# Performance work log

Hardware: AMD Instinct MI355X
Metric: run time of the kernel (lower is better)

Reference implementation:

```python
import math
import jax, jax.numpy as jnp
import numpy as np

N_HEADS = 12


def _rel_to_abs(x):
    # x: [b, h, L, 2L-1] relative logits -> [b, h, L, L] absolute-position scores
    b, h, L, _ = x.shape
    x = jnp.pad(x, ((0, 0), (0, 0), (0, 0), (0, 1)))           # [b,h,L,2L]
    xf = x.reshape(b, h, L * 2 * L)
    xf = jnp.pad(xf, ((0, 0), (0, 0), (0, L - 1)))
    return xf.reshape(b, h, L + 1, 2 * L - 1)[:, :, :L, L - 1:]


def _abs_to_rel(x):
    # x: [b, h, L, L] attention weights -> [b, h, L, 2L-1] relative-position weights
    b, h, L, _ = x.shape
    x = jnp.pad(x, ((0, 0), (0, 0), (0, 0), (0, L - 1)))        # [b,h,L,2L-1]
    xf = x.reshape(b, h, L * (2 * L - 1))
    xf = jnp.pad(xf, ((0, 0), (0, 0), (L, 0)))
    return xf.reshape(b, h, L, 2 * L)[:, :, :, 1:]


def _get_relative_embeddings(emb, length):
    # emb: [n_rel, 2*window+1, k] -> [n_rel, 2*length-1, k]
    window = (emb.shape[1] - 1) // 2
    pad_len = max(length - (window + 1), 0)
    start = max(window + 1 - length, 0)
    if pad_len > 0:
        emb = jnp.pad(emb, ((0, 0), (pad_len, pad_len), (0, 0)))
    return emb[:, start:start + 2 * length - 1]


def setup_inputs() -> dict:
    key = jax.random.key(0)
    ks = jax.random.split(key, 8)
    B, C, T, H = 4, 768, 1024, N_HEADS
    K = C // H
    W = 10
    xavier = math.sqrt(2.0 / (C + C))          # xavier_uniform std analogue
    rel_std = K ** (-0.5)
    return {
        "x": jax.random.normal(ks[0], (B, C, T), jnp.float32),
        "c": jax.random.normal(ks[1], (B, C, T), jnp.float32),
        "Wq": jax.random.normal(ks[2], (C, C), jnp.float32) * xavier,
        "bq": jnp.zeros((C,), jnp.float32),
        "Wk": jax.random.normal(ks[3], (C, C), jnp.float32) * xavier,
        "bk": jnp.zeros((C,), jnp.float32),
        "Wv": jax.random.normal(ks[4], (C, C), jnp.float32) * xavier,
        "bv": jnp.zeros((C,), jnp.float32),
        "Wo": jax.random.normal(ks[5], (C, C), jnp.float32) * xavier,
        "bo": jnp.zeros((C,), jnp.float32),
        "emb_rel_k": jax.random.normal(ks[6], (1, 2 * W + 1, K), jnp.float32) * rel_std,
        "emb_rel_v": jax.random.normal(ks[7], (1, 2 * W + 1, K), jnp.float32) * rel_std,
    }


def reference(x, c, Wq, bq, Wk, bk, Wv, bv, Wo, bo, emb_rel_k, emb_rel_v):
    B, C, T = x.shape
    H = N_HEADS
    K = C // H

    def proj(W_, b_, inp):  # Conv1d(kernel=1) == channel-wise linear
        return jnp.einsum('oi,bit->bot', W_, inp) + b_[None, :, None]

    # [B,C,T] -> [B,H,T,K]
    q = proj(Wq, bq, x).reshape(B, H, K, T).transpose(0, 1, 3, 2)
    k = proj(Wk, bk, c).reshape(B, H, K, T).transpose(0, 1, 3, 2)
    v = proj(Wv, bv, c).reshape(B, H, K, T).transpose(0, 1, 3, 2)

    qs = q * (1.0 / math.sqrt(K))
    scores = jnp.einsum('bhtd,bhsd->bhts', qs, k)               # [B,H,T,T]

    # relative key logits via skewing trick
    rel_k = _get_relative_embeddings(emb_rel_k, T)              # [1,2T-1,K]
    rel_logits = jnp.einsum('bhtd,md->bhtm', qs, rel_k[0])      # [B,H,T,2T-1]
    scores = scores + _rel_to_abs(rel_logits)

    # proximal bias: -log(1 + |i - j|)
    r = jnp.arange(T, dtype=scores.dtype)
    scores = scores - jnp.log1p(jnp.abs(r[None, :] - r[:, None]))[None, None]

    p = jax.nn.softmax(scores, axis=-1)
    out = jnp.einsum('bhts,bhsd->bhtd', p, v)                   # [B,H,T,K]

    # relative value contribution
    rel_v = _get_relative_embeddings(emb_rel_v, T)              # [1,2T-1,K]
    out = out + jnp.einsum('bhtm,md->bhtd', _abs_to_rel(p), rel_v[0])

    out = out.transpose(0, 1, 3, 2).reshape(B, C, T)            # [B,C,T]
    return jnp.einsum('oi,bit->bot', Wo, out) + bo[None, :, None]
```

## Files before the change

### kernel.cpp

```cpp
#include <hip/hip_runtime.h>
#include <hip/hip_bf16.h>

using bf16 = __hip_bfloat16;
typedef __attribute__((ext_vector_type(8))) short short8;
typedef __attribute__((ext_vector_type(4))) float f32x4;

static constexpr int C = 768, T = 1024, H = 12, D = 64;

__device__ __forceinline__ f32x4 mfma16(short8 a, short8 b, f32x4 c){
  return __builtin_amdgcn_mfma_f32_16x16x32_bf16(a, b, c, 0, 0, 0);
}

__device__ __forceinline__ void gload16(const void* g, void* l){
  void* gv = const_cast<void*>(g);
  __builtin_amdgcn_global_load_lds((__attribute__((address_space(1))) void*)gv,
                                   (__attribute__((address_space(3))) void*)l, 16, 0, 0);
}

__device__ __forceinline__ float b2f(short s){
  unsigned u = ((unsigned)(unsigned short)s) << 16;
  return __builtin_bit_cast(float, u);
}

__device__ __forceinline__ int cvtpk(float a, float b){
  int r;
  asm("v_cvt_pk_bf16_f32 %0, %1, %2" : "=v"(r) : "v"(a), "v"(b));
  return r;
}

union PkU { int i[4]; short8 v; };

__global__ __launch_bounds__(256) void prep_kernel(const float* __restrict__ xin,
    const float* __restrict__ cin, const float* __restrict__ Wq,
    const float* __restrict__ Wk, const float* __restrict__ Wv,
    const float* __restrict__ Wo, bf16* __restrict__ xo, bf16* __restrict__ co,
    bf16* __restrict__ wq, bf16* __restrict__ wk, bf16* __restrict__ wv,
    bf16* __restrict__ wo){
  const int z = blockIdx.z;
  if (z < 8){
    __shared__ float tile[64][65];
    const int b = z & 3, which = z >> 2;
    const float* in = which ? cin : xin;
    bf16* out = which ? co : xo;
    const int t0 = blockIdx.x*64, c0 = blockIdx.y*64;
    const int u = threadIdx.x & 63, r0 = threadIdx.x >> 6;
    const float* ip = in + ((size_t)b*C + c0)*T + t0;
    #pragma unroll
    for (int i = r0; i < 64; i += 4) tile[i][u] = ip[(size_t)i*T + u];
    __syncthreads();
    bf16* op = out + ((size_t)b*T + t0)*C + c0;
    #pragma unroll
    for (int j = r0; j < 64; j += 4) op[(size_t)j*C + u] = (bf16)tile[u][j];
  } else {
    const int chunk = (z - 8)*192 + blockIdx.y*16 + blockIdx.x;
    const int m = chunk / 576;
    const int off = (chunk % 576)*1024 + threadIdx.x*4;
    const float* in = m==0 ? Wq : m==1 ? Wk : m==2 ? Wv : Wo;
    bf16* out = m==0 ? wq : m==1 ? wk : m==2 ? wv : wo;
    float4 v = *(const float4*)(in + off);
    out[off+0] = (bf16)v.x; out[off+1] = (bf16)v.y;
    out[off+2] = (bf16)v.z; out[off+3] = (bf16)v.w;
  }
}

__global__ __launch_bounds__(256,3) void gemm_qkv(const bf16* __restrict__ xb,
    const bf16* __restrict__ cb, const bf16* __restrict__ wq, const bf16* __restrict__ wk,
    const bf16* __restrict__ wv, const float* __restrict__ bq, const float* __restrict__ bk,
    const float* __restrict__ bv, bf16* __restrict__ qout, bf16* __restrict__ kout,
    bf16* __restrict__ vout){
  const int tid = threadIdx.x, lane = tid & 63, w = tid >> 6;
  const int wr = w >> 1, wc = w & 1, g = lane >> 4, cl = lane & 15;
  const int bz = blockIdx.y, b = bz & 3, mode = bz >> 2;
  const int lb = blockIdx.x;
  int m0, n0;
  if (mode == 2){ m0 = (lb >> 3)*128; n0 = (lb & 7)*128; }
  else          { m0 = (lb & 7)*128;  n0 = (lb >> 3)*128; }
  const bf16* A  = (mode==0) ? xb + (size_t)b*T*C : (mode==1) ? cb + (size_t)b*T*C : wv;
  const bf16* Bp = (mode==2) ? cb + (size_t)b*T*C : (mode==0) ? wq : wk;
  const float* bias = (mode==0) ? bq : (mode==1) ? bk : bv;
  const float scale = (mode==0) ? 0.125f*1.44269504088896f : 1.0f;
  __shared__ bf16 lA[128*64], lB[128*64];
  f32x4 acc[4][4] = {};
  const bf16* Ars = A  + (size_t)m0*768;
  const bf16* Brs = Bp + (size_t)n0*768;
  for (int k0 = 0; k0 < 768; k0 += 64){
    __syncthreads();
    #pragma unroll
    for (int rr = 0; rr < 4; ++rr){
      const int u = rr*256 + tid;
      const int row = u >> 3, cc = u & 7;
      const int src = row*768 + k0 + ((cc ^ (row & 7))*8);
      gload16(Ars + src, &lA[(size_t)u*8]);
      gload16(Brs + src, &lB[(size_t)u*8]);
    }
    __syncthreads();
    #pragma unroll
    for (int kh = 0; kh < 2; ++kh){
      short8 af[4], bfr[4];
      #pragma unroll
      for (int mi = 0; mi < 4; ++mi){
        const int row = wr*64 + mi*16 + cl;
        af[mi] = *(const short8*)&lA[row*64 + (((g + kh*4) ^ (row & 7))*8)];
      }
      #pragma unroll
      for (int ni = 0; ni < 4; ++ni){
        const int row = wc*64 + ni*16 + cl;
        bfr[ni] = *(const short8*)&lB[row*64 + (((g + kh*4) ^ (row & 7))*8)];
      }
      __builtin_amdgcn_s_setprio(1);
      #pragma unroll
      for (int mi = 0; mi < 4; ++mi)
        #pragma unroll
        for (int ni = 0; ni < 4; ++ni)
          acc[mi][ni] = mfma16(af[mi], bfr[ni], acc[mi][ni]);
      __builtin_amdgcn_s_setprio(0);
    }
  }
  #pragma unroll
  for (int mi = 0; mi < 4; ++mi){
    const int mB = m0 + wr*64 + mi*16 + g*4;
    #pragma unroll
    for (int ni = 0; ni < 4; ++ni){
      const int n = n0 + wc*64 + ni*16 + cl;
      #pragma unroll
      for (int r = 0; r < 4; ++r){
        const int m = mB + r;
        float v = acc[mi][ni][r];
        if (mode <= 1){
          v = (v + bias[n]) * scale;
          bf16* outp = mode ? kout : qout;
          outp[(size_t)b*(H*T*D) + (size_t)(n >> 6)*(T*D) + (size_t)m*D + (n & 63)] = (bf16)v;
        } else {
          v += bias[m];
          vout[(size_t)b*(C*T) + (size_t)m*T + n] = (bf16)v;
        }
      }
    }
  }
}

__global__ __launch_bounds__(256,3) void gemm_o(const bf16* __restrict__ wo,
                                                const bf16* __restrict__ attn,
                                                const float* __restrict__ bias,
                                                float* __restrict__ outp){
  const int tid = threadIdx.x, lane = tid & 63, w = tid >> 6;
  const int wr = w >> 1, wc = w & 1, g = lane >> 4, cl = lane & 15;
  const int b = blockIdx.z;
  const int q = blockIdx.y*6 + blockIdx.x;
  const int m0 = (q >> 3)*128, n0 = (q & 7)*128;
  __shared__ bf16 lA[128*64], lB[128*64];
  f32x4 acc[4][4] = {};
  const bf16* Ars = wo + (size_t)m0*768;
  const bf16* Brs = attn + (size_t)b*T*C + (size_t)n0*768;
  for (int k0 = 0; k0 < 768; k0 += 64){
    __syncthreads();
    #pragma unroll
    for (int rr = 0; rr < 4; ++rr){
      const int u = rr*256 + tid;
      const int row = u >> 3, cc = u & 7;
      const int src = row*768 + k0 + ((cc ^ (row & 7))*8);
      gload16(Ars + src, &lA[(size_t)u*8]);
      gload16(Brs + src, &lB[(size_t)u*8]);
    }
    __syncthreads();
    #pragma unroll
    for (int kh = 0; kh < 2; ++kh){
      short8 af[4], bfr[4];
      #pragma unroll
      for (int mi = 0; mi < 4; ++mi){
        const int row = wr*64 + mi*16 + cl;
        af[mi] = *(const short8*)&lA[row*64 + (((g + kh*4) ^ (row & 7))*8)];
      }
      #pragma unroll
      for (int ni = 0; ni < 4; ++ni){
        const int row = wc*64 + ni*16 + cl;
        bfr[ni] = *(const short8*)&lB[row*64 + (((g + kh*4) ^ (row & 7))*8)];
      }
      __builtin_amdgcn_s_setprio(1);
      #pragma unroll
      for (int mi = 0; mi < 4; ++mi)
        #pragma unroll
        for (int ni = 0; ni < 4; ++ni)
          acc[mi][ni] = mfma16(af[mi], bfr[ni], acc[mi][ni]);
      __builtin_amdgcn_s_setprio(0);
    }
  }
  #pragma unroll
  for (int mi = 0; mi < 4; ++mi){
    const int mB = m0 + wr*64 + mi*16 + g*4;
    #pragma unroll
    for (int ni = 0; ni < 4; ++ni){
      const int n = n0 + wc*64 + ni*16 + cl;
      #pragma unroll
      for (int r = 0; r < 4; ++r){
        const int m = mB + r;
        outp[(size_t)b*(C*T) + (size_t)m*T + n] = acc[mi][ni][r] + bias[m];
      }
    }
  }
}

__global__ __launch_bounds__(256,4) void attn_kernel(const bf16* __restrict__ qws,
                                                     const bf16* __restrict__ kws,
                                                     const bf16* __restrict__ vws,
                                                     bf16* __restrict__ aws,
                                                     const float* __restrict__ relk,
                                                     const float* __restrict__ relv){
  const int tid = threadIdx.x, lane = tid & 63, w = tid >> 6;
  const int g = lane >> 4, cl = lane & 15;
  const int i0 = blockIdx.y*64, bh = blockIdx.x;
  const int b = bh / H, h = bh % H;
  const int ql = w*16 + cl;
  const int qt = i0 + ql;

  __shared__ __align__(16) char smem[40960];
  bf16*  lKV   = (bf16*)smem;
  float* bandS = (float*)(smem + 32768);
  bf16*  relkD = (bf16*)(smem + 38144);
  bf16*  lEmb32 = lKV + 4096;
  bf16*  lEV    = lKV;
  bf16*  lQ     = lKV + 3*4096;

  const bf16* qg = qws + ((size_t)bh*T + i0)*D;
  const bf16* kg = kws + (size_t)bh*T*D;
  const bf16* vg = vws + ((size_t)b*C + h*D)*T;

  int kOff[2], vOff[2], qOff[2], dst[2];
  #pragma unroll
  for (int r = 0; r < 2; ++r){
    const int u = r*256 + tid, L = u >> 3, cc = u & 7;
    const int sc8 = (cc ^ (L & 7))*8;
    const int sig = (((L>>4)&1)<<5) | (((L>>2)&3)<<3) | (((L>>5)&1)<<2) | (L&3);
    kOff[r] = sig*64 + sc8;
    vOff[r] = L*T + sc8;
    qOff[r] = L*64 + sc8;
    dst[r]  = u*8;
  }

  #pragma unroll
  for (int r = 0; r < 2; ++r){
    gload16(qg + qOff[r], &lQ[dst[r]]);
    gload16(kg + kOff[r], &lKV[dst[r]]);
    gload16(vg + vOff[r], &lKV[2*4096 + dst[r]]);
  }
  for (int idx = tid; idx < 2048; idx += 256){
    const int row = idx >> 6, col = idx & 63;
    const float v = (row < 21) ? relk[idx] : 0.0f;
    lEmb32[row*64 + (((col >> 3) ^ (row & 7))*8) + (col & 7)] = (bf16)v;
  }
  __syncthreads();

  const short8 aq0 = *(const short8*)&lQ[ql*64 + ((g ^ (ql & 7))*8)];
  const short8 aq1 = *(const short8*)&lQ[ql*64 + (((g + 4) ^ (ql & 7))*8)];

  #pragma unroll
  for (int ni2 = 0; ni2 < 2; ++ni2){
    const int row = ni2*16 + cl;
    short8 e0 = *(const short8*)&lEmb32[row*64 + ((g ^ (row & 7))*8)];
    short8 e1 = *(const short8*)&lEmb32[row*64 + (((g + 4) ^ (row & 7))*8)];
    f32x4 rk = {};
    rk = mfma16(e0, aq0, rk);
    rk = mfma16(e1, aq1, rk);
    #pragma unroll
    for (int rr = 0; rr < 4; ++rr){
      const int ridx = ni2*16 + 4*g + rr;
      if (ridx < 21) relkD[ql*22 + ridx] = (bf16)rk[rr];
    }
  }
  __syncthreads();

  float mreg = -1e30f, lreg = 0.f;
  f32x4 o[4] = {};
  const int koffA[4] = {8*g, 32 + 8*g, 4 + 8*g, 36 + 8*g};

  for (int jt = 0; jt < 16; ++jt){
    const int j0 = jt*64, cur = jt & 1, nxt = cur ^ 1;
    if (jt < 15){
      const int jn = j0 + 64;
      #pragma unroll
      for (int r = 0; r < 2; ++r){
        gload16(kg + jn*64 + kOff[r], &lKV[nxt*4096 + dst[r]]);
        gload16(vg + jn + vOff[r],    &lKV[(2 + nxt)*4096 + dst[r]]);
      }
      asm volatile("s_waitcnt vmcnt(4)" ::: "memory");
    } else {
      asm volatile("s_waitcnt vmcnt(0)" ::: "memory");
    }
    asm volatile("s_barrier" ::: "memory");

    const bf16* Kc = lKV + cur*4096;
    const bf16* Vc = lKV + (2 + cur)*4096;

    f32x4 s[4] = {};
    __builtin_amdgcn_s_setprio(1);
    #pragma unroll
    for (int ni = 0; ni < 4; ++ni){
      const int row = ni*16 + cl;
      short8 k0f = *(const short8*)&Kc[row*64 + ((g ^ (row & 7))*8)];
      s[ni] = mfma16(k0f, aq0, s[ni]);
      short8 k1f = *(const short8*)&Kc[row*64 + (((g + 4) ^ (row & 7))*8)];
      s[ni] = mfma16(k1f, aq1, s[ni]);
    }
    __builtin_amdgcn_s_setprio(0);

    const int dj = j0 - i0;
    if (dj == 0 || dj == 64 || dj == -64){
      #pragma unroll
      for (int ni = 0; ni < 4; ++ni){
        const int ibase = j0 + koffA[ni] - qt;
        #pragma unroll
        for (int r = 0; r < 4; ++r){
          const int dd = ibase + r;
          float v = s[ni][r] - __log2f(fabsf((float)dd) + 1.0f);
          if ((unsigned)(dd + 10) <= 20u){
            v += b2f(*(const short*)&relkD[ql*22 + dd + 10]);
            bandS[ql*21 + dd + 10] = v;
          }
          s[ni][r] = v;
        }
      }
    } else {
      #pragma unroll
      for (int ni = 0; ni < 4; ++ni){
        const float fb = (float)(j0 + koffA[ni] - qt);
        #pragma unroll
        for (int r = 0; r < 4; ++r)
          s[ni][r] -= __log2f(fabsf(fb + (float)r) + 1.0f);
      }
    }

    float m0 = fmaxf(fmaxf(s[0][0], s[0][1]), fmaxf(s[0][2], s[0][3]));
    float m1 = fmaxf(fmaxf(s[1][0], s[1][1]), fmaxf(s[1][2], s[1][3]));
    float m2 = fmaxf(fmaxf(s[2][0], s[2][1]), fmaxf(s[2][2], s[2][3]));
    float m3 = fmaxf(fmaxf(s[3][0], s[3][1]), fmaxf(s[3][2], s[3][3]));
    float mx = fmaxf(fmaxf(m0, m1), fmaxf(m2, m3));
    mx = fmaxf(mx, __shfl_xor(mx, 16));
    mx = fmaxf(mx, __shfl_xor(mx, 32));
    if (!__all(mx <= mreg + 8.0f)){
      const float mn = fmaxf(mreg, mx);
      const float sc = __builtin_amdgcn_exp2f(mreg - mn);
      lreg *= sc;
      #pragma unroll
      for (int di = 0; di < 4; ++di)
        #pragma unroll
        for (int r = 0; r < 4; ++r) o[di][r] *= sc;
      mreg = mn;
    }
    float rs = 0.f;
    #pragma unroll
    for (int ni = 0; ni < 4; ++ni)
      #pragma unroll
      for (int r = 0; r < 4; ++r){
        float p = __builtin_amdgcn_exp2f(s[ni][r] - mreg);
        s[ni][r] = p; rs += p;
      }
    rs += __shfl_xor(rs, 16);
    rs += __shfl_xor(rs, 32);
    lreg += rs;

    PkU bf0, bf1;
    bf0.i[0] = cvtpk(s[0][0], s[0][1]); bf0.i[1] = cvtpk(s[0][2], s[0][3]);
    bf0.i[2] = cvtpk(s[2][0], s[2][1]); bf0.i[3] = cvtpk(s[2][2], s[2][3]);
    bf1.i[0] = cvtpk(s[1][0], s[1][1]); bf1.i[1] = cvtpk(s[1][2], s[1][3]);
    bf1.i[2] = cvtpk(s[3][0], s[3][1]); bf1.i[3] = cvtpk(s[3][2], s[3][3]);

    __builtin_amdgcn_s_setprio(1);
    #pragma unroll
    for (int di = 0; di < 4; ++di){
      const int vrow = di*16 + cl;
      short8 a0 = *(const short8*)&Vc[vrow*64 + ((g ^ (vrow & 7))*8)];
      o[di] = mfma16(a0, bf0.v, o[di]);
      short8 a1 = *(const short8*)&Vc[vrow*64 + (((g + 4) ^ (vrow & 7))*8)];
      o[di] = mfma16(a1, bf1.v, o[di]);
    }
    __builtin_amdgcn_s_setprio(0);
    asm volatile("s_barrier" ::: "memory");
  }

  for (int idx = tid; idx < 2048; idx += 256){
    const int d = idx >> 5, c = idx & 31;
    const float v = (c < 21) ? relv[c*64 + d] : 0.0f;
    lEV[d*32 + (((c >> 3) ^ ((d >> 2) & 3))*8) + (c & 7)] = (bf16)v;
  }
  __syncthreads();

  const float invl = 1.0f / lreg;
  float pb[8];
  #pragma unroll
  for (int e = 0; e < 8; ++e){
    const int ddi = 8*g + e;
    float pv = 0.f;
    if (ddi < 21){
      const int j = qt + ddi - 10;
      if (j >= 0 && j < T)
        pv = __builtin_amdgcn_exp2f(bandS[ql*21 + ddi] - mreg) * invl;
    }
    pb[e] = pv;
  }
  PkU bfE;
  bfE.i[0] = cvtpk(pb[0], pb[1]); bfE.i[1] = cvtpk(pb[2], pb[3]);
  bfE.i[2] = cvtpk(pb[4], pb[5]); bfE.i[3] = cvtpk(pb[6], pb[7]);

  bf16* outp = aws + (size_t)(b*T + qt)*C + h*64;
  #pragma unroll
  for (int di = 0; di < 4; ++di){
    const int arow = di*16 + cl;
    short8 aE = *(const short8*)&lEV[arow*32 + ((g ^ ((arow >> 2) & 3))*8)];
    f32x4 z = {};
    f32x4 ba = mfma16(aE, bfE.v, z);
    const int p0 = cvtpk(o[di][0]*invl + ba[0], o[di][1]*invl + ba[1]);
    const int p1 = cvtpk(o[di][2]*invl + ba[2], o[di][3]*invl + ba[3]);
    *(int2*)(outp + di*16 + 4*g) = make_int2(p0, p1);
  }
}

extern "C" void kernel_launch(void* const* d_in, const int* in_sizes, int n_in,
                              void* d_out, int out_size, void* d_ws, size_t ws_size,
                              hipStream_t stream){
  const float* x    = (const float*)d_in[0];
  const float* cin  = (const float*)d_in[1];
  const float* Wq   = (const float*)d_in[2];
  const float* bq   = (const float*)d_in[3];
  const float* Wk   = (const float*)d_in[4];
  const float* bk   = (const float*)d_in[5];
  const float* Wv   = (const float*)d_in[6];
  const float* bv   = (const float*)d_in[7];
  const float* Wo   = (const float*)d_in[8];
  const float* bo   = (const float*)d_in[9];
  const float* relk = (const float*)d_in[10];
  const float* relv = (const float*)d_in[11];

  char* ws = (char*)d_ws;
  constexpr size_t SZ_W = (size_t)768*768*2;
  constexpr size_t SZ_T = (size_t)4*1024*768*2;
  bf16* wq  = (bf16*)(ws + 0*SZ_W);
  bf16* wk  = (bf16*)(ws + 1*SZ_W);
  bf16* wv  = (bf16*)(ws + 2*SZ_W);
  bf16* wo  = (bf16*)(ws + 3*SZ_W);
  bf16* xb  = (bf16*)(ws + 4*SZ_W);
  bf16* cb  = (bf16*)(ws + 4*SZ_W + 1*SZ_T);
  bf16* qws = (bf16*)(ws + 4*SZ_W + 2*SZ_T);
  bf16* kws = (bf16*)(ws + 4*SZ_W + 3*SZ_T);
  bf16* vws = (bf16*)(ws + 4*SZ_W + 4*SZ_T);
  bf16* attn = xb;

  prep_kernel<<<dim3(16,12,20), 256, 0, stream>>>(x, cin, Wq, Wk, Wv, Wo,
                                                  xb, cb, wq, wk, wv, wo);
  gemm_qkv<<<dim3(48,12), 256, 0, stream>>>(xb, cb, wq, wk, wv, bq, bk, bv, qws, kws, vws);
  attn_kernel<<<dim3(48,16), 256, 0, stream>>>(qws, kws, vws, attn, relk, relv);
  gemm_o<<<dim3(6,8,4), 256, 0, stream>>>(wo, attn, bo, (float*)d_out);
}
```

Before: 93.82 us.

## Stream K tiles into registers instead of LDS and shrink shared memory

K fragments are now read straight from global memory into registers, with the next tile prefetched during the current tile's softmax and PV work. Only V stays double-buffered in LDS, and the LDS footprint shrinks by reusing buffers for Q, the embedding staging and the V tiles. This removes the LDS write and read traffic for K. In exchange it raises register pressure, so launch bounds drop from 4 to 3 blocks per CU, and the strided direct global loads may coalesce less well.

```diff
diff --git a/kernel.cpp b/kernel.cpp
--- a/kernel.cpp
+++ b/kernel.cpp
@@ -200,7 +200,7 @@
   }
 }
 
-__global__ __launch_bounds__(256,4) void attn_kernel(const bf16* __restrict__ qws,
+__global__ __launch_bounds__(256,3) void attn_kernel(const bf16* __restrict__ qws,
                                                      const bf16* __restrict__ kws,
                                                      const bf16* __restrict__ vws,
                                                      bf16* __restrict__ aws,
@@ -213,40 +213,51 @@
   const int ql = w*16 + cl;
   const int qt = i0 + ql;
 
-  __shared__ __align__(16) char smem[40960];
-  bf16*  lKV   = (bf16*)smem;
-  float* bandS = (float*)(smem + 32768);
-  bf16*  relkD = (bf16*)(smem + 38144);
-  bf16*  lEmb32 = lKV + 4096;
-  bf16*  lEV    = lKV;
-  bf16*  lQ     = lKV + 3*4096;
+  __shared__ __align__(16) char smem[24576];
+  bf16*  vb0   = (bf16*)smem;
+  bf16*  vb1   = (bf16*)(smem + 8192);
+  float* bandS = (float*)(smem + 16384);
+  bf16*  relkD = (bf16*)(smem + 21760);
+  bf16*  lEmb32 = (bf16*)(smem + 16384);
+  bf16*  lQ     = vb1;
+  bf16*  lEV    = vb0;
 
   const bf16* qg = qws + ((size_t)bh*T + i0)*D;
   const bf16* kg = kws + (size_t)bh*T*D;
   const bf16* vg = vws + ((size_t)b*C + h*D)*T;
 
-  int kOff[2], vOff[2], qOff[2], dst[2];
+  int vOff[2], qOff[2], dst[2];
   #pragma unroll
   for (int r = 0; r < 2; ++r){
     const int u = r*256 + tid, L = u >> 3, cc = u & 7;
     const int sc8 = (cc ^ (L & 7))*8;
-    const int sig = (((L>>4)&1)<<5) | (((L>>2)&3)<<3) | (((L>>5)&1)<<2) | (L&3);
-    kOff[r] = sig*64 + sc8;
     vOff[r] = L*T + sc8;
     qOff[r] = L*64 + sc8;
     dst[r]  = u*8;
   }
+  int koff[4];
+  #pragma unroll
+  for (int ni = 0; ni < 4; ++ni){
+    const int row = ni*16 + cl;
+    const int sigr = (((row>>4)&1)<<5) | (((row>>2)&3)<<3) | (((row>>5)&1)<<2) | (row&3);
+    koff[ni] = sigr*64 + g*8;
+  }
 
   #pragma unroll
   for (int r = 0; r < 2; ++r){
     gload16(qg + qOff[r], &lQ[dst[r]]);
-    gload16(kg + kOff[r], &lKV[dst[r]]);
-    gload16(vg + vOff[r], &lKV[2*4096 + dst[r]]);
+    gload16(vg + vOff[r], &vb0[dst[r]]);
   }
   for (int idx = tid; idx < 2048; idx += 256){
     const int row = idx >> 6, col = idx & 63;
     const float v = (row < 21) ? relk[idx] : 0.0f;
     lEmb32[row*64 + (((col >> 3) ^ (row & 7))*8) + (col & 7)] = (bf16)v;
+  }
+  short8 kr[4][2];
+  #pragma unroll
+  for (int ni = 0; ni < 4; ++ni){
+    kr[ni][0] = *(const short8*)(kg + koff[ni]);
+    kr[ni][1] = *(const short8*)(kg + koff[ni] + 32);
   }
   __syncthreads();
 
@@ -274,34 +285,37 @@
   const int koffA[4] = {8*g, 32 + 8*g, 4 + 8*g, 36 + 8*g};
 
   for (int jt = 0; jt < 16; ++jt){
-    const int j0 = jt*64, cur = jt & 1, nxt = cur ^ 1;
+    const int j0 = jt*64, cur = jt & 1;
     if (jt < 15){
-      const int jn = j0 + 64;
-      #pragma unroll
-      for (int r = 0; r < 2; ++r){
-        gload16(kg + jn*64 + kOff[r], &lKV[nxt*4096 + dst[r]]);
-        gload16(vg + jn + vOff[r],    &lKV[(2 + nxt)*4096 + dst[r]]);
-      }
-      asm volatile("s_waitcnt vmcnt(4)" ::: "memory");
+      const bf16* vgn = vg + j0 + 64;
+      bf16* vdst = cur ? vb0 : vb1;
+      gload16(vgn + vOff[0], &vdst[dst[0]]);
+      gload16(vgn + vOff[1], &vdst[dst[1]]);
+      asm volatile("s_waitcnt vmcnt(2)" ::: "memory");
     } else {
       asm volatile("s_waitcnt vmcnt(0)" ::: "memory");
     }
     asm volatile("s_barrier" ::: "memory");
 
-    const bf16* Kc = lKV + cur*4096;
-    const bf16* Vc = lKV + (2 + cur)*4096;
-
-    f32x4 s[4] = {};
+    f32x4 s[4];
     __builtin_amdgcn_s_setprio(1);
     #pragma unroll
     for (int ni = 0; ni < 4; ++ni){
-      const int row = ni*16 + cl;
-      short8 k0f = *(const short8*)&Kc[row*64 + ((g ^ (row & 7))*8)];
-      s[ni] = mfma16(k0f, aq0, s[ni]);
-      short8 k1f = *(const short8*)&Kc[row*64 + (((g + 4) ^ (row & 7))*8)];
-      s[ni] = mfma16(k1f, aq1, s[ni]);
+      f32x4 a = {};
+      a = mfma16(kr[ni][0], aq0, a);
+      a = mfma16(kr[ni][1], aq1, a);
+      s[ni] = a;
     }
     __builtin_amdgcn_s_setprio(0);
+
+    if (jt < 15){
+      const bf16* kgn = kg + (size_t)(j0 + 64)*64;
+      #pragma unroll
+      for (int ni = 0; ni < 4; ++ni){
+        kr[ni][0] = *(const short8*)(kgn + koff[ni]);
+        kr[ni][1] = *(const short8*)(kgn + koff[ni] + 32);
+      }
+    }
 
     const int dj = j0 - i0;
     if (dj == 0 || dj == 64 || dj == -64){
@@ -364,6 +378,7 @@
     bf1.i[0] = cvtpk(s[1][0], s[1][1]); bf1.i[1] = cvtpk(s[1][2], s[1][3]);
     bf1.i[2] = cvtpk(s[3][0], s[3][1]); bf1.i[3] = cvtpk(s[3][2], s[3][3]);
 
+    const bf16* Vc = cur ? vb1 : vb0;
     __builtin_amdgcn_s_setprio(1);
     #pragma unroll
     for (int di = 0; di < 4; ++di){
```

New measurement: 111.4 us. 18.8% more time.
